# Kernel optimization log

Measured on AMD Instinct MI355X. Metric: run time of the kernel, lower is better.

## Reference

```python
import jax, jax.numpy as jnp
import numpy as np
import math

C_IN, C_OUT = 256, 256
KH, KW = 3, 3
STRIDE, PAD = 1, 1
CURV = 1.0
SQRT_C = math.sqrt(CURV)
EPS = 1e-15

def _beta(a, b):
    return math.exp(math.lgamma(a) + math.lgamma(b) - math.lgamma(a + b))

BETA_NI = _beta(C_IN / 2.0, 0.5)                 # beta(n_i/2, 1/2)
BETA_N = _beta(C_IN * KH * KW / 2.0, 0.5)        # beta(n/2, 1/2)


def logmap0(y, axis):
    n = jnp.maximum(jnp.linalg.norm(y, axis=axis, keepdims=True), EPS)
    return jnp.arctanh(jnp.minimum(SQRT_C * n, 1.0 - 1e-7)) * y / (SQRT_C * n)


def expmap0(v, axis):
    n = jnp.maximum(jnp.linalg.norm(v, axis=axis, keepdims=True), EPS)
    return jnp.tanh(SQRT_C * n) * v / (SQRT_C * n)


def unfold(x):
    # torch.nn.Unfold: x [B,C,H,W] -> [B, C*KH*KW, L], channel-major patch order
    B, C, H, W = x.shape
    Ho = (H + 2 * PAD - KH) // STRIDE + 1
    Wo = (W + 2 * PAD - KW) // STRIDE + 1
    xp = jnp.pad(x, ((0, 0), (0, 0), (PAD, PAD), (PAD, PAD)))
    cols = [xp[:, :, i:i + STRIDE * Ho:STRIDE, j:j + STRIDE * Wo:STRIDE]
            for i in range(KH) for j in range(KW)]
    patches = jnp.stack(cols, axis=2)            # [B, C, KH*KW, Ho, Wo]
    return patches.reshape(B, C * KH * KW, Ho * Wo), Ho, Wo


def poincare_fc(x, z, r):
    # x: [..., D_in] on ball, z: [D_in, D_out], r: [D_out]
    x2 = jnp.sum(x * x, axis=-1, keepdims=True)
    lam = 2.0 / (1.0 - CURV * x2)                # conformal factor lambda_x
    z_norm = jnp.maximum(jnp.linalg.norm(z, axis=0), EPS)  # [D_out]
    xz = x @ z                                   # [..., D_out]
    two_csr = 2.0 * SQRT_C * r
    inner = (SQRT_C * lam * xz / z_norm * jnp.cosh(two_csr)
             - (lam - 1.0) * jnp.sinh(two_csr))
    v = 2.0 * z_norm / SQRT_C * jnp.arcsinh(inner)   # hyperplane distances
    w = jnp.sinh(SQRT_C * v) / SQRT_C
    return w / (1.0 + jnp.sqrt(1.0 + CURV * jnp.sum(w * w, axis=-1, keepdims=True)))


def setup_inputs() -> dict:
    key = jax.random.key(0)
    k1, k2, k3 = jax.random.split(key, 3)
    # tangent vectors -> points on the Poincare ball (man_dim=1)
    v = 0.05 * jax.random.normal(k1, (16, C_IN, 64, 64), dtype=jnp.float32)
    x = expmap0(v, axis=1)
    std = (2.0 * C_IN * KH * KW * C_OUT) ** (-0.5)
    weights = std * jax.random.normal(k2, (KH * KW * C_IN, C_OUT), dtype=jnp.float32)
    bias = 0.01 * jax.random.normal(k3, (C_OUT,), dtype=jnp.float32)
    return {"x": x, "weights": weights, "bias": bias}


def reference(x, weights, bias):
    B = x.shape[0]
    v = logmap0(x, axis=1) * (BETA_N / BETA_NI)      # log map + beta scaling
    u, Ho, Wo = unfold(v)                            # [B, CK, L]
    u = jnp.swapaxes(u, 1, 2)                        # [B, L, CK]
    p = expmap0(u, axis=-1)                          # back onto the ball
    y = poincare_fc(p, weights, bias)                # [B, L, C_OUT]
    return jnp.swapaxes(y, 1, 2).reshape(B, C_OUT, Ho, Wo)
```

## Files before the change

### kernel.cpp

```cpp
#include <hip/hip_runtime.h>
#include <cmath>

typedef __bf16 bf16;
typedef __bf16 bf16x8 __attribute__((ext_vector_type(8)));
typedef float f32x4 __attribute__((ext_vector_type(4)));

#define SBAR() __builtin_amdgcn_sched_barrier(0)


__device__ inline void gload16(const void* g, void* l) {
    __builtin_amdgcn_global_load_lds(
        (const __attribute__((address_space(1))) unsigned int*)g,
        (__attribute__((address_space(3))) unsigned int*)l, 16, 0, 0);
}

__global__ void k_prep_zt(const float* __restrict__ z, bf16* __restrict__ zt5) {
    int s = blockIdx.x;
    int cc = s / 9, tap = s % 9;
    int co = threadIdx.x;
#pragma unroll
    for (int g = 0; g < 4; ++g) {
        bf16x8 pk;
#pragma unroll
        for (int e = 0; e < 8; ++e) {
            int c = cc * 32 + g * 8 + e;
            pk[e] = (bf16)z[(size_t)(c * 9 + tap) * 256 + co];
        }
        *(bf16x8*)(zt5 + ((size_t)(s * 4 + g) * 256 + co) * 8) = pk;
    }
}

__global__ void k_prep_cols(const float* __restrict__ z, const float* __restrict__ r,
                            float* __restrict__ zn, float* __restrict__ ch,
                            float* __restrict__ sh) {
    __shared__ float red[256];
    int co = blockIdx.x, t = threadIdx.x;
    float s = 0.f;
    for (int i = 0; i < 9; ++i) {
        float v = z[(size_t)(i * 256 + t) * 256 + co];
        s += v * v;
    }
    red[t] = s;
    __syncthreads();
    for (int off = 128; off >= 1; off >>= 1) {
        if (t < off) red[t] += red[t + off];
        __syncthreads();
    }
    if (t == 0) {
        zn[co] = fmaxf(sqrtf(red[0]), 1e-15f);
        float tc = 2.f * r[co];
        ch[co] = coshf(tc);
        sh[co] = sinhf(tc);
    }
}

__global__ void k_logmap(const float* __restrict__ x, unsigned int* __restrict__ vt_u,
                         float* __restrict__ sq, float Rbeta) {
    __shared__ float tile[256][33];
    __shared__ float red[8][32];
    __shared__ float afac[32];
    int tid = threadIdx.x;
    int blk = blockIdx.x;
    int b = blk >> 7;
    int pix0 = (blk & 127) << 5;

    for (int it = 0; it < 32; ++it) {
        int c = it * 8 + (tid >> 5);
        int p = tid & 31;
        tile[c][p] = x[((size_t)b * 256 + c) * 4096 + pix0 + p];
    }
    __syncthreads();

    {
        int part = tid >> 5, p = tid & 31;
        float s = 0.f;
        for (int i = 0; i < 32; ++i) {
            float v = tile[part * 32 + i][p];
            s += v * v;
        }
        red[part][p] = s;
    }
    __syncthreads();
    if (tid < 32) {
        float n2 = 0.f;
        for (int i = 0; i < 8; ++i) n2 += red[i][tid];
        float n = sqrtf(n2);
        float nc = fmaxf(n, 1e-15f);
        float a = atanhf(fminf(nc, 0.9999999f)) / nc * Rbeta;
        afac[tid] = a;
        sq[(size_t)b * 4096 + pix0 + tid] = a * a * n2;
    }
    __syncthreads();

    for (int it = 0; it < 16; ++it) {
        int idx = it * 256 + tid;
        int p = idx >> 7;
        int cp = idx & 127;
        float a = afac[p];
        float v0 = a * tile[2 * cp][p];
        float v1 = a * tile[2 * cp + 1][p];
        union { bf16 h[2]; unsigned int u; } pk;
        pk.h[0] = (bf16)v0;
        pk.h[1] = (bf16)v1;
        vt_u[((size_t)b * 4096 + pix0 + p) * 128 + cp] = pk.u;
    }
}

__global__ void k_boxsum(const float* __restrict__ sq, float* __restrict__ nusq) {
    int idx = blockIdx.x * 256 + threadIdx.x;
    int b = idx >> 12, hw = idx & 4095, h = hw >> 6, w = hw & 63;
    const float* s = sq + ((size_t)b << 12);
    float acc = 0.f;
    for (int dh = -1; dh <= 1; ++dh) {
        int hh = h + dh;
        if ((unsigned)hh >= 64u) continue;
        for (int dw = -1; dw <= 1; ++dw) {
            int ww = w + dw;
            if ((unsigned)ww >= 64u) continue;
            acc += s[hh * 64 + ww];
        }
    }
    nusq[idx] = acc;
}

__global__ void
__attribute__((amdgpu_flat_work_group_size(512, 512)))
__attribute__((amdgpu_waves_per_eu(4, 4)))
k_hconv(const bf16* __restrict__ vt, const bf16* __restrict__ zt5,
        const float* __restrict__ nusq,
        const float* __restrict__ znp, const float* __restrict__ chp,
        const float* __restrict__ shp, float* __restrict__ out) {
    __shared__ __align__(1024) char Asb[16896];
    __shared__ __align__(1024) char Bsb[3][16448];
    __shared__ float s_lds[128], lam_lds[128];
    __shared__ float red[128][4];

    int tid = threadIdx.x;
    int bid = blockIdx.x;
    int bh = ((bid & 7) << 6) | (bid >> 3);
    int b = bh >> 5, h0 = (bh & 31) << 1;

    if (tid < 32) {
        int u = tid >> 1, side = tid & 1;
        *(f32x4*)(Asb + u * 1056 + side * 1040) = (f32x4){0.f, 0.f, 0.f, 0.f};
    }

    if (tid >= 128 && tid < 256) {
        int t = tid - 128;
        int h = h0 + (t >> 6), w = t & 63;
        float q = nusq[((size_t)b << 12) + h * 64 + w];
        float ncl = fmaxf(sqrtf(q), 1e-15f);
        float p = __expf(2.f * ncl);
        float tt = (p - 1.f) / (p + 1.f);
        s_lds[t] = tt / ncl;
        lam_lds[t] = 2.f / (1.f - tt * tt);
    }

    int wave = tid >> 6, lane = tid & 63;
    int wn = wave & 3, wm = wave >> 2;
    int lrow = lane & 15, lk = lane >> 4;

    f32x4 acc[4][4];
#pragma unroll
    for (int m = 0; m < 4; ++m)
#pragma unroll
        for (int n = 0; n < 4; ++n) acc[m][n] = (f32x4){0.f, 0.f, 0.f, 0.f};

    const bf16* vb = vt + (((size_t)b) << 12) * 256;

    auto stageA = [&](int ccn) {
#pragma unroll
        for (int it = 0; it < 2; ++it) {
            int u = wave * 2 + it;
            int r = u >> 2, g = u & 3;
            int hr = h0 - 1 + r;
            hr = hr < 0 ? 0 : (hr > 63 ? 63 : hr);
            const bf16* gp = vb + ((size_t)(hr * 64 + lane)) * 256 + ccn * 32 + g * 8;
            gload16(gp, Asb + u * 1056 + 16);
        }
    };
    auto stageB = [&](char* dst, int snext) {
        const char* src = (const char*)zt5 + (size_t)snext * 16384;
#pragma unroll
        for (int it = 0; it < 2; ++it) {
            int u = wave * 2 + it;
            gload16(src + u * 1024 + lane * 16,
                    dst + (u >> 2) * 4112 + (u & 3) * 1024);
        }
    };

    stageB((char*)Bsb[0], 0);
    stageA(0);
    __syncthreads();
    SBAR();

    const char* ApB = Asb + lk * 1056 + lrow * 16;
    const int bOff = lk * 4112 + wn * 1024 + lrow * 16;

#pragma unroll 1
    for (int cc = 0; cc < 8; ++cc) {
        const int sbase = cc * 9;
        const bool notlast = (cc < 7);

#pragma unroll
        for (int tap = 0; tap < 9; ++tap) {
            const int s = sbase + tap;
            if (s < 71) stageB((char*)Bsb[(tap + 1) % 3], s + 1);
            SBAR();
            if (s < 71) { asm volatile("s_waitcnt vmcnt(2)" ::: "memory"); }
            else        { asm volatile("s_waitcnt vmcnt(0)" ::: "memory"); }
            SBAR();
            asm volatile("s_barrier" ::: "memory");
            SBAR();

            const int dh = tap / 3 - 1, dw = tap % 3 - 1;
            int hh = h0 + wm + dh;
            if ((unsigned)hh < 64u) {
                const char* Ap = ApB + (wm + dh + 1) * 4224 + (dw + 1) * 16;
                const char* Bp = (const char*)Bsb[tap % 3] + bOff;
                bf16x8 a0 = *(const bf16x8*)(Ap);
                bf16x8 a1 = *(const bf16x8*)(Ap + 256);
                bf16x8 a2 = *(const bf16x8*)(Ap + 512);
                bf16x8 a3 = *(const bf16x8*)(Ap + 768);
                bf16x8 b0 = *(const bf16x8*)(Bp);
                bf16x8 b1 = *(const bf16x8*)(Bp + 256);
                bf16x8 b2 = *(const bf16x8*)(Bp + 512);
                bf16x8 b3 = *(const bf16x8*)(Bp + 768);
                __builtin_amdgcn_s_setprio(1);
                acc[0][0] = __builtin_amdgcn_mfma_f32_16x16x32_bf16(a0, b0, acc[0][0], 0, 0, 0);
                acc[1][0] = __builtin_amdgcn_mfma_f32_16x16x32_bf16(a1, b0, acc[1][0], 0, 0, 0);
                acc[2][0] = __builtin_amdgcn_mfma_f32_16x16x32_bf16(a2, b0, acc[2][0], 0, 0, 0);
                acc[3][0] = __builtin_amdgcn_mfma_f32_16x16x32_bf16(a3, b0, acc[3][0], 0, 0, 0);
                acc[0][1] = __builtin_amdgcn_mfma_f32_16x16x32_bf16(a0, b1, acc[0][1], 0, 0, 0);
                acc[1][1] = __builtin_amdgcn_mfma_f32_16x16x32_bf16(a1, b1, acc[1][1], 0, 0, 0);
                acc[2][1] = __builtin_amdgcn_mfma_f32_16x16x32_bf16(a2, b1, acc[2][1], 0, 0, 0);
                acc[3][1] = __builtin_amdgcn_mfma_f32_16x16x32_bf16(a3, b1, acc[3][1], 0, 0, 0);
                acc[0][2] = __builtin_amdgcn_mfma_f32_16x16x32_bf16(a0, b2, acc[0][2], 0, 0, 0);
                acc[1][2] = __builtin_amdgcn_mfma_f32_16x16x32_bf16(a1, b2, acc[1][2], 0, 0, 0);
                acc[2][2] = __builtin_amdgcn_mfma_f32_16x16x32_bf16(a2, b2, acc[2][2], 0, 0, 0);
                acc[3][2] = __builtin_amdgcn_mfma_f32_16x16x32_bf16(a3, b2, acc[3][2], 0, 0, 0);
                acc[0][3] = __builtin_amdgcn_mfma_f32_16x16x32_bf16(a0, b3, acc[0][3], 0, 0, 0);
                acc[1][3] = __builtin_amdgcn_mfma_f32_16x16x32_bf16(a1, b3, acc[1][3], 0, 0, 0);
                acc[2][3] = __builtin_amdgcn_mfma_f32_16x16x32_bf16(a2, b3, acc[2][3], 0, 0, 0);
                acc[3][3] = __builtin_amdgcn_mfma_f32_16x16x32_bf16(a3, b3, acc[3][3], 0, 0, 0);
                __builtin_amdgcn_s_setprio(0);
            }
            SBAR();
            if (tap == 8) {
                asm volatile("s_barrier" ::: "memory");
                SBAR();
                if (notlast) stageA(cc + 1);
                SBAR();
            }
        }
    }

    float cz[4], sh4[4], tz[4];
#pragma unroll
    for (int n = 0; n < 4; ++n) {
        int co = wn * 64 + n * 16 + lrow;
        float zn = znp[co];
        cz[n] = chp[co] / zn;
        sh4[n] = shp[co];
        tz[n] = 2.f * zn;
    }

#pragma unroll
    for (int m = 0; m < 4; ++m) {
#pragma unroll
        for (int r = 0; r < 4; ++r) {
            int wp = wm * 64 + m * 16 + 4 * lk + r;
            float s = s_lds[wp], lam = lam_lds[wp];
            float lm1 = lam - 1.f;
            float psum = 0.f;
#pragma unroll
            for (int n = 0; n < 4; ++n) {
                float xz = s * acc[m][n][r];
                float inner = lam * xz * cz[n] - lm1 * sh4[n];
                float as = __logf(inner + sqrtf(inner * inner + 1.f));
                float p = __expf(tz[n] * as);
                float w = 0.5f * (p - __builtin_amdgcn_rcpf(p));
                acc[m][n][r] = w;
                psum += w * w;
            }
            psum += __shfl_xor(psum, 1);
            psum += __shfl_xor(psum, 2);
            psum += __shfl_xor(psum, 4);
            psum += __shfl_xor(psum, 8);
            if (lrow == 0) red[wp][wn] = psum;
        }
    }
    __syncthreads();

    float dinv[4][4];
#pragma unroll
    for (int m = 0; m < 4; ++m)
#pragma unroll
        for (int r = 0; r < 4; ++r) {
            int wp = wm * 64 + m * 16 + 4 * lk + r;
            float tot = (red[wp][0] + red[wp][1]) + (red[wp][2] + red[wp][3]);
            dinv[m][r] = __builtin_amdgcn_rcpf(1.f + sqrtf(1.f + tot));
        }

    float* ob = out + (size_t)b * 256 * 4096 + (h0 + wm) * 64;
#pragma unroll
    for (int m = 0; m < 4; ++m) {
#pragma unroll
        for (int n = 0; n < 4; ++n) {
            int co = wn * 64 + n * 16 + lrow;
            f32x4 o;
#pragma unroll
            for (int r = 0; r < 4; ++r) o[r] = acc[m][n][r] * dinv[m][r];
            *(f32x4*)(ob + (size_t)co * 4096 + m * 16 + 4 * lk) = o;
        }
    }
}

extern "C" void kernel_launch(void* const* d_in, const int* in_sizes, int n_in,
                              void* d_out, int out_size, void* d_ws, size_t ws_size,
                              hipStream_t stream) {
    const float* x = (const float*)d_in[0];
    const float* z = (const float*)d_in[1];
    const float* r = (const float*)d_in[2];
    float* out = (float*)d_out;

    char* ws = (char*)d_ws;
    bf16* vt = (bf16*)ws;
    float* sq = (float*)(ws + 33554432);
    float* nusq = (float*)(ws + 33816576);
    bf16* zt5 = (bf16*)(ws + 34078720);
    float* zn = (float*)(ws + 35258368);
    float* ch = (float*)(ws + 35259392);
    float* sh = (float*)(ws + 35260416);
    if (ws_size < 35261440) return;

    double bni = lgamma(128.0) + lgamma(0.5) - lgamma(128.5);
    double bn = lgamma(1152.0) + lgamma(0.5) - lgamma(1152.5);
    float Rbeta = (float)exp(bn - bni);

    k_prep_zt<<<72, 256, 0, stream>>>(z, zt5);
    k_prep_cols<<<256, 256, 0, stream>>>(z, r, zn, ch, sh);
    k_logmap<<<2048, 256, 0, stream>>>(x, (unsigned int*)vt, sq, Rbeta);
    k_boxsum<<<256, 256, 0, stream>>>(sq, nusq);
    k_hconv<<<512, 512, 0, stream>>>(vt, zt5, nusq, zn, ch, sh, out);
}
```

Before: 127.3 us.

## Load conv A operands directly from global in channel-group-blocked layout, dropping LDS staging

The logmap kernel now writes activations in a channel-group-blocked layout ([B][32 groups][pixel][8 channels]), so each MFMA lane can fetch its 16-byte A fragment straight from global memory. The conv kernel removes the A shared-memory tile and its extra barrier per channel chunk. It prefetches the next tap's A fragments into registers, with border pixels handled by masking lanes to zero. This trades LDS traffic and a sync for more global/L2 loads (each element is re-read across taps) and more vmcnt bookkeeping, and it also pads the B LDS stride differently.

```diff
diff --git a/kernel.cpp b/kernel.cpp
--- a/kernel.cpp
+++ b/kernel.cpp
@@ -94,15 +94,17 @@
 
     for (int it = 0; it < 16; ++it) {
         int idx = it * 256 + tid;
-        int p = idx >> 7;
-        int cp = idx & 127;
+        int q = idx & 3;
+        int p = (idx >> 2) & 31;
+        int g = idx >> 7;
+        int cp = g * 4 + q;
         float a = afac[p];
         float v0 = a * tile[2 * cp][p];
         float v1 = a * tile[2 * cp + 1][p];
         union { bf16 h[2]; unsigned int u; } pk;
         pk.h[0] = (bf16)v0;
         pk.h[1] = (bf16)v1;
-        vt_u[((size_t)b * 4096 + pix0 + p) * 128 + cp] = pk.u;
+        vt_u[((size_t)(b * 32 + g) * 4096 + pix0 + p) * 4 + q] = pk.u;
     }
 }
 
@@ -126,12 +128,11 @@
 __global__ void
 __attribute__((amdgpu_flat_work_group_size(512, 512)))
 __attribute__((amdgpu_waves_per_eu(4, 4)))
-k_hconv(const bf16* __restrict__ vt, const bf16* __restrict__ zt5,
+k_hconv(const bf16* __restrict__ vt2, const bf16* __restrict__ zt5,
         const float* __restrict__ nusq,
         const float* __restrict__ znp, const float* __restrict__ chp,
         const float* __restrict__ shp, float* __restrict__ out) {
-    __shared__ __align__(1024) char Asb[16896];
-    __shared__ __align__(1024) char Bsb[3][16448];
+    __shared__ __align__(1024) char Bsb[3][16512];
     __shared__ float s_lds[128], lam_lds[128];
     __shared__ float red[128][4];
 
@@ -140,20 +141,14 @@
     int bh = ((bid & 7) << 6) | (bid >> 3);
     int b = bh >> 5, h0 = (bh & 31) << 1;
 
-    if (tid < 32) {
-        int u = tid >> 1, side = tid & 1;
-        *(f32x4*)(Asb + u * 1056 + side * 1040) = (f32x4){0.f, 0.f, 0.f, 0.f};
-    }
-
-    if (tid >= 128 && tid < 256) {
-        int t = tid - 128;
-        int h = h0 + (t >> 6), w = t & 63;
+    if (tid < 128) {
+        int h = h0 + (tid >> 6), w = tid & 63;
         float q = nusq[((size_t)b << 12) + h * 64 + w];
         float ncl = fmaxf(sqrtf(q), 1e-15f);
         float p = __expf(2.f * ncl);
         float tt = (p - 1.f) / (p + 1.f);
-        s_lds[t] = tt / ncl;
-        lam_lds[t] = 2.f / (1.f - tt * tt);
+        s_lds[tid] = tt / ncl;
+        lam_lds[tid] = 2.f / (1.f - tt * tt);
     }
 
     int wave = tid >> 6, lane = tid & 63;
@@ -166,49 +161,66 @@
 #pragma unroll
         for (int n = 0; n < 4; ++n) acc[m][n] = (f32x4){0.f, 0.f, 0.f, 0.f};
 
-    const bf16* vb = vt + (((size_t)b) << 12) * 256;
-
-    auto stageA = [&](int ccn) {
+    bf16x8 zf;
+#pragma unroll
+    for (int e = 0; e < 8; ++e) zf[e] = (bf16)0.0f;
+
+    const bf16* Aptr[3];
+#pragma unroll
+    for (int j = 0; j < 3; ++j) {
+        int hj = h0 + wm - 1 + j;
+        hj = hj < 0 ? 0 : (hj > 63 ? 63 : hj);
+        Aptr[j] = vt2 + (size_t)(b * 32 + lk) * 32768 + hj * 512 + lrow * 8;
+    }
+    const int dL = (lrow == 0) ? 0 : -16;
+    const bool okL = (lrow != 0);
+    const bool okR = (lrow != 15);
+
+    auto stageB = [&](char* dst, int snext) {
 #pragma unroll
         for (int it = 0; it < 2; ++it) {
             int u = wave * 2 + it;
-            int r = u >> 2, g = u & 3;
-            int hr = h0 - 1 + r;
-            hr = hr < 0 ? 0 : (hr > 63 ? 63 : hr);
-            const bf16* gp = vb + ((size_t)(hr * 64 + lane)) * 256 + ccn * 32 + g * 8;
-            gload16(gp, Asb + u * 1056 + 16);
+            gload16((const char*)zt5 + (size_t)snext * 16384 + u * 1024 + lane * 16,
+                    dst + (u >> 2) * 4128 + (u & 3) * 1024);
         }
     };
-    auto stageB = [&](char* dst, int snext) {
-        const char* src = (const char*)zt5 + (size_t)snext * 16384;
-#pragma unroll
-        for (int it = 0; it < 2; ++it) {
-            int u = wave * 2 + it;
-            gload16(src + u * 1024 + lane * 16,
-                    dst + (u >> 2) * 4112 + (u & 3) * 1024);
-        }
-    };
 
     stageB((char*)Bsb[0], 0);
-    stageA(0);
+    bf16x8 ap[4];
+#pragma unroll
+    for (int m = 0; m < 4; ++m)
+        ap[m] = (m == 0) ? *(const bf16x8*)((const char*)Aptr[0] + dL)
+                         : *(const bf16x8*)(Aptr[0] + (m * 16 - 1) * 8);
     __syncthreads();
     SBAR();
 
-    const char* ApB = Asb + lk * 1056 + lrow * 16;
-    const int bOff = lk * 4112 + wn * 1024 + lrow * 16;
+    const int bOff = lk * 4128 + wn * 1024 + lrow * 16;
 
 #pragma unroll 1
     for (int cc = 0; cc < 8; ++cc) {
-        const int sbase = cc * 9;
-        const bool notlast = (cc < 7);
-
 #pragma unroll
         for (int tap = 0; tap < 9; ++tap) {
-            const int s = sbase + tap;
-            if (s < 71) stageB((char*)Bsb[(tap + 1) % 3], s + 1);
+            const int s = cc * 9 + tap;
+            const bool lastS = (s == 71);
+
+            if (tap == 8) {
+#pragma unroll
+                for (int j = 0; j < 3; ++j) Aptr[j] += 4 * 32768;
+            }
+            if (!lastS) stageB((char*)Bsb[(tap + 1) % 3], s + 1);
+            bf16x8 an[4];
+            {
+                const int nt = (tap == 8) ? 0 : tap + 1;
+                const int ndh = nt / 3 - 1, ndw = nt % 3 - 1, nj = ndh + 1;
+#pragma unroll
+                for (int m = 0; m < 4; ++m)
+                    an[m] = (ndw == -1 && m == 0)
+                        ? *(const bf16x8*)((const char*)Aptr[nj] + dL)
+                        : *(const bf16x8*)(Aptr[nj] + (m * 16 + ndw) * 8);
+            }
             SBAR();
-            if (s < 71) { asm volatile("s_waitcnt vmcnt(2)" ::: "memory"); }
-            else        { asm volatile("s_waitcnt vmcnt(0)" ::: "memory"); }
+            if (!lastS) { asm volatile("s_waitcnt vmcnt(6)" ::: "memory"); }
+            else        { asm volatile("s_waitcnt vmcnt(4)" ::: "memory"); }
             SBAR();
             asm volatile("s_barrier" ::: "memory");
             SBAR();
@@ -216,12 +228,10 @@
             const int dh = tap / 3 - 1, dw = tap % 3 - 1;
             int hh = h0 + wm + dh;
             if ((unsigned)hh < 64u) {
-                const char* Ap = ApB + (wm + dh + 1) * 4224 + (dw + 1) * 16;
+                bf16x8 a0 = ap[0], a1 = ap[1], a2 = ap[2], a3 = ap[3];
+                if (dw == -1) a0 = okL ? a0 : zf;
+                if (dw == 1)  a3 = okR ? a3 : zf;
                 const char* Bp = (const char*)Bsb[tap % 3] + bOff;
-                bf16x8 a0 = *(const bf16x8*)(Ap);
-                bf16x8 a1 = *(const bf16x8*)(Ap + 256);
-                bf16x8 a2 = *(const bf16x8*)(Ap + 512);
-                bf16x8 a3 = *(const bf16x8*)(Ap + 768);
                 bf16x8 b0 = *(const bf16x8*)(Bp);
                 bf16x8 b1 = *(const bf16x8*)(Bp + 256);
                 bf16x8 b2 = *(const bf16x8*)(Bp + 512);
@@ -246,12 +256,8 @@
                 __builtin_amdgcn_s_setprio(0);
             }
             SBAR();
-            if (tap == 8) {
-                asm volatile("s_barrier" ::: "memory");
-                SBAR();
-                if (notlast) stageA(cc + 1);
-                SBAR();
-            }
+#pragma unroll
+            for (int m = 0; m < 4; ++m) ap[m] = an[m];
         }
     }
 
@@ -325,7 +331,7 @@
     float* out = (float*)d_out;
 
     char* ws = (char*)d_ws;
-    bf16* vt = (bf16*)ws;
+    bf16* vt2 = (bf16*)ws;
     float* sq = (float*)(ws + 33554432);
     float* nusq = (float*)(ws + 33816576);
     bf16* zt5 = (bf16*)(ws + 34078720);
@@ -340,7 +346,7 @@
 
     k_prep_zt<<<72, 256, 0, stream>>>(z, zt5);
     k_prep_cols<<<256, 256, 0, stream>>>(z, r, zn, ch, sh);
-    k_logmap<<<2048, 256, 0, stream>>>(x, (unsigned int*)vt, sq, Rbeta);
+    k_logmap<<<2048, 256, 0, stream>>>(x, (unsigned int*)vt2, sq, Rbeta);
     k_boxsum<<<256, 256, 0, stream>>>(sq, nusq);
-    k_hconv<<<512, 512, 0, stream>>>(vt, zt5, nusq, zn, ch, sh, out);
-}
+    k_hconv<<<512, 512, 0, stream>>>(vt2, zt5, nusq, zn, ch, sh, out);
+}
```

Result: slower. 141.0 us (+10.8%).

## Load weight fragments directly into registers, dropping LDS B staging and per-tap barriers

Applied to the files above, without the earlier changes.

The weight matrix is re-laid out so each lane's four k-groups are contiguous, and the conv kernel now loads its B fragments straight from global memory into double-buffered registers instead of staging them through a triple-buffered LDS ring. This removes the per-tap workgroup barrier and the B LDS traffic. Barriers remain only at channel-chunk boundaries for the A tile. In exchange, every wave issues its own global/L2 reads of the weights, and register pressure rises under the fixed 4-waves-per-EU budget.

```diff
diff --git a/kernel.cpp b/kernel.cpp
--- a/kernel.cpp
+++ b/kernel.cpp
@@ -14,7 +14,7 @@
         (__attribute__((address_space(3))) unsigned int*)l, 16, 0, 0);
 }
 
-__global__ void k_prep_zt(const float* __restrict__ z, bf16* __restrict__ zt5) {
+__global__ void k_prep_zt(const float* __restrict__ z, bf16* __restrict__ zt6) {
     int s = blockIdx.x;
     int cc = s / 9, tap = s % 9;
     int co = threadIdx.x;
@@ -26,7 +26,7 @@
             int c = cc * 32 + g * 8 + e;
             pk[e] = (bf16)z[(size_t)(c * 9 + tap) * 256 + co];
         }
-        *(bf16x8*)(zt5 + ((size_t)(s * 4 + g) * 256 + co) * 8) = pk;
+        *(bf16x8*)(zt6 + ((size_t)(s * 256 + co) * 4 + g) * 8) = pk;
     }
 }
 
@@ -126,12 +126,11 @@
 __global__ void
 __attribute__((amdgpu_flat_work_group_size(512, 512)))
 __attribute__((amdgpu_waves_per_eu(4, 4)))
-k_hconv(const bf16* __restrict__ vt, const bf16* __restrict__ zt5,
+k_hconv(const bf16* __restrict__ vt, const bf16* __restrict__ zt6,
         const float* __restrict__ nusq,
         const float* __restrict__ znp, const float* __restrict__ chp,
         const float* __restrict__ shp, float* __restrict__ out) {
     __shared__ __align__(1024) char Asb[16896];
-    __shared__ __align__(1024) char Bsb[3][16448];
     __shared__ float s_lds[128], lam_lds[128];
     __shared__ float red[128][4];
 
@@ -179,81 +178,85 @@
             gload16(gp, Asb + u * 1056 + 16);
         }
     };
-    auto stageB = [&](char* dst, int snext) {
-        const char* src = (const char*)zt5 + (size_t)snext * 16384;
-#pragma unroll
-        for (int it = 0; it < 2; ++it) {
-            int u = wave * 2 + it;
-            gload16(src + u * 1024 + lane * 16,
-                    dst + (u >> 2) * 4112 + (u & 3) * 1024);
-        }
-    };
-
-    stageB((char*)Bsb[0], 0);
+
+    const bf16* bp = zt6 + ((size_t)(wn * 64 + lrow) * 4 + lk) * 8;
+    bf16x8 bA[4], bB[4];
+#pragma unroll
+    for (int n = 0; n < 4; ++n) bA[n] = *(const bf16x8*)(bp + n * 512);
+    const bf16* bnp = bp + 8192;
+
     stageA(0);
     __syncthreads();
     SBAR();
 
     const char* ApB = Asb + lk * 1056 + lrow * 16;
-    const int bOff = lk * 4112 + wn * 1024 + lrow * 16;
+
+#define STAGE(CCV, TAP, CUR, NXT)                                            \
+    {                                                                        \
+        const int s_ = (CCV) * 9 + (TAP);                                    \
+        if (s_ < 71) {                                                       \
+            NXT[0] = *(const bf16x8*)(bnp);                                  \
+            NXT[1] = *(const bf16x8*)(bnp + 512);                            \
+            NXT[2] = *(const bf16x8*)(bnp + 1024);                           \
+            NXT[3] = *(const bf16x8*)(bnp + 1536);                           \
+            bnp += 8192;                                                     \
+        }                                                                    \
+        SBAR();                                                              \
+        if ((TAP) == 0) {                                                    \
+            asm volatile("s_waitcnt vmcnt(4)" ::: "memory");                 \
+            SBAR();                                                          \
+            asm volatile("s_barrier" ::: "memory");         \
+            SBAR();                                                          \
+        }                                                                    \
+        {                                                                    \
+            const int dh_ = (TAP) / 3 - 1, dw_ = (TAP) % 3 - 1;              \
+            int hh_ = h0 + wm + dh_;                                         \
+            if ((unsigned)hh_ < 64u) {                                       \
+                const char* Ap_ = ApB + (wm + dh_ + 1) * 4224 + (dw_ + 1) * 16; \
+                bf16x8 a0 = *(const bf16x8*)(Ap_);                           \
+                bf16x8 a1 = *(const bf16x8*)(Ap_ + 256);                     \
+                bf16x8 a2 = *(const bf16x8*)(Ap_ + 512);                     \
+                bf16x8 a3 = *(const bf16x8*)(Ap_ + 768);                     \
+                __builtin_amdgcn_s_setprio(1);                               \
+                acc[0][0] = __builtin_amdgcn_mfma_f32_16x16x32_bf16(a0, CUR[0], acc[0][0], 0, 0, 0); \
+                acc[1][0] = __builtin_amdgcn_mfma_f32_16x16x32_bf16(a1, CUR[0], acc[1][0], 0, 0, 0); \
+                acc[2][0] = __builtin_amdgcn_mfma_f32_16x16x32_bf16(a2, CUR[0], acc[2][0], 0, 0, 0); \
+                acc[3][0] = __builtin_amdgcn_mfma_f32_16x16x32_bf16(a3, CUR[0], acc[3][0], 0, 0, 0); \
+                acc[0][1] = __builtin_amdgcn_mfma_f32_16x16x32_bf16(a0, CUR[1], acc[0][1], 0, 0, 0); \
+                acc[1][1] = __builtin_amdgcn_mfma_f32_16x16x32_bf16(a1, CUR[1], acc[1][1], 0, 0, 0); \
+                acc[2][1] = __builtin_amdgcn_mfma_f32_16x16x32_bf16(a2, CUR[1], acc[2][1], 0, 0, 0); \
+                acc[3][1] = __builtin_amdgcn_mfma_f32_16x16x32_bf16(a3, CUR[1], acc[3][1], 0, 0, 0); \
+                acc[0][2] = __builtin_amdgcn_mfma_f32_16x16x32_bf16(a0, CUR[2], acc[0][2], 0, 0, 0); \
+                acc[1][2] = __builtin_amdgcn_mfma_f32_16x16x32_bf16(a1, CUR[2], acc[1][2], 0, 0, 0); \
+                acc[2][2] = __builtin_amdgcn_mfma_f32_16x16x32_bf16(a2, CUR[2], acc[2][2], 0, 0, 0); \
+                acc[3][2] = __builtin_amdgcn_mfma_f32_16x16x32_bf16(a3, CUR[2], acc[3][2], 0, 0, 0); \
+                acc[0][3] = __builtin_amdgcn_mfma_f32_16x16x32_bf16(a0, CUR[3], acc[0][3], 0, 0, 0); \
+                acc[1][3] = __builtin_amdgcn_mfma_f32_16x16x32_bf16(a1, CUR[3], acc[1][3], 0, 0, 0); \
+                acc[2][3] = __builtin_amdgcn_mfma_f32_16x16x32_bf16(a2, CUR[3], acc[2][3], 0, 0, 0); \
+                acc[3][3] = __builtin_amdgcn_mfma_f32_16x16x32_bf16(a3, CUR[3], acc[3][3], 0, 0, 0); \
+                __builtin_amdgcn_s_setprio(0);                               \
+            }                                                                \
+        }                                                                    \
+        SBAR();                                                              \
+        if ((TAP) == 8 && (CCV) < 7) {                                       \
+            asm volatile("s_barrier" ::: "memory");    \
+            SBAR();                                                          \
+            stageA((CCV) + 1);                                               \
+            SBAR();                                                          \
+        }                                                                    \
+    }
 
 #pragma unroll 1
-    for (int cc = 0; cc < 8; ++cc) {
-        const int sbase = cc * 9;
-        const bool notlast = (cc < 7);
-
-#pragma unroll
-        for (int tap = 0; tap < 9; ++tap) {
-            const int s = sbase + tap;
-            if (s < 71) stageB((char*)Bsb[(tap + 1) % 3], s + 1);
-            SBAR();
-            if (s < 71) { asm volatile("s_waitcnt vmcnt(2)" ::: "memory"); }
-            else        { asm volatile("s_waitcnt vmcnt(0)" ::: "memory"); }
-            SBAR();
-            asm volatile("s_barrier" ::: "memory");
-            SBAR();
-
-            const int dh = tap / 3 - 1, dw = tap % 3 - 1;
-            int hh = h0 + wm + dh;
-            if ((unsigned)hh < 64u) {
-                const char* Ap = ApB + (wm + dh + 1) * 4224 + (dw + 1) * 16;
-                const char* Bp = (const char*)Bsb[tap % 3] + bOff;
-                bf16x8 a0 = *(const bf16x8*)(Ap);
-                bf16x8 a1 = *(const bf16x8*)(Ap + 256);
-                bf16x8 a2 = *(const bf16x8*)(Ap + 512);
-                bf16x8 a3 = *(const bf16x8*)(Ap + 768);
-                bf16x8 b0 = *(const bf16x8*)(Bp);
-                bf16x8 b1 = *(const bf16x8*)(Bp + 256);
-                bf16x8 b2 = *(const bf16x8*)(Bp + 512);
-                bf16x8 b3 = *(const bf16x8*)(Bp + 768);
-                __builtin_amdgcn_s_setprio(1);
-                acc[0][0] = __builtin_amdgcn_mfma_f32_16x16x32_bf16(a0, b0, acc[0][0], 0, 0, 0);
-                acc[1][0] = __builtin_amdgcn_mfma_f32_16x16x32_bf16(a1, b0, acc[1][0], 0, 0, 0);
-                acc[2][0] = __builtin_amdgcn_mfma_f32_16x16x32_bf16(a2, b0, acc[2][0], 0, 0, 0);
-                acc[3][0] = __builtin_amdgcn_mfma_f32_16x16x32_bf16(a3, b0, acc[3][0], 0, 0, 0);
-                acc[0][1] = __builtin_amdgcn_mfma_f32_16x16x32_bf16(a0, b1, acc[0][1], 0, 0, 0);
-                acc[1][1] = __builtin_amdgcn_mfma_f32_16x16x32_bf16(a1, b1, acc[1][1], 0, 0, 0);
-                acc[2][1] = __builtin_amdgcn_mfma_f32_16x16x32_bf16(a2, b1, acc[2][1], 0, 0, 0);
-                acc[3][1] = __builtin_amdgcn_mfma_f32_16x16x32_bf16(a3, b1, acc[3][1], 0, 0, 0);
-                acc[0][2] = __builtin_amdgcn_mfma_f32_16x16x32_bf16(a0, b2, acc[0][2], 0, 0, 0);
-                acc[1][2] = __builtin_amdgcn_mfma_f32_16x16x32_bf16(a1, b2, acc[1][2], 0, 0, 0);
-                acc[2][2] = __builtin_amdgcn_mfma_f32_16x16x32_bf16(a2, b2, acc[2][2], 0, 0, 0);
-                acc[3][2] = __builtin_amdgcn_mfma_f32_16x16x32_bf16(a3, b2, acc[3][2], 0, 0, 0);
-                acc[0][3] = __builtin_amdgcn_mfma_f32_16x16x32_bf16(a0, b3, acc[0][3], 0, 0, 0);
-                acc[1][3] = __builtin_amdgcn_mfma_f32_16x16x32_bf16(a1, b3, acc[1][3], 0, 0, 0);
-                acc[2][3] = __builtin_amdgcn_mfma_f32_16x16x32_bf16(a2, b3, acc[2][3], 0, 0, 0);
-                acc[3][3] = __builtin_amdgcn_mfma_f32_16x16x32_bf16(a3, b3, acc[3][3], 0, 0, 0);
-                __builtin_amdgcn_s_setprio(0);
-            }
-            SBAR();
-            if (tap == 8) {
-                asm volatile("s_barrier" ::: "memory");
-                SBAR();
-                if (notlast) stageA(cc + 1);
-                SBAR();
-            }
-        }
-    }
+    for (int cc2 = 0; cc2 < 4; ++cc2) {
+        const int c0 = cc2 * 2, c1 = c0 + 1;
+        STAGE(c0, 0, bA, bB) STAGE(c0, 1, bB, bA) STAGE(c0, 2, bA, bB)
+        STAGE(c0, 3, bB, bA) STAGE(c0, 4, bA, bB) STAGE(c0, 5, bB, bA)
+        STAGE(c0, 6, bA, bB) STAGE(c0, 7, bB, bA) STAGE(c0, 8, bA, bB)
+        STAGE(c1, 0, bB, bA) STAGE(c1, 1, bA, bB) STAGE(c1, 2, bB, bA)
+        STAGE(c1, 3, bA, bB) STAGE(c1, 4, bB, bA) STAGE(c1, 5, bA, bB)
+        STAGE(c1, 6, bB, bA) STAGE(c1, 7, bA, bB) STAGE(c1, 8, bB, bA)
+    }
+#undef STAGE
 
     float cz[4], sh4[4], tz[4];
 #pragma unroll
@@ -328,7 +331,7 @@
     bf16* vt = (bf16*)ws;
     float* sq = (float*)(ws + 33554432);
     float* nusq = (float*)(ws + 33816576);
-    bf16* zt5 = (bf16*)(ws + 34078720);
+    bf16* zt6 = (bf16*)(ws + 34078720);
     float* zn = (float*)(ws + 35258368);
     float* ch = (float*)(ws + 35259392);
     float* sh = (float*)(ws + 35260416);
@@ -338,9 +341,9 @@
     double bn = lgamma(1152.0) + lgamma(0.5) - lgamma(1152.5);
     float Rbeta = (float)exp(bn - bni);
 
-    k_prep_zt<<<72, 256, 0, stream>>>(z, zt5);
+    k_prep_zt<<<72, 256, 0, stream>>>(z, zt6);
     k_prep_cols<<<256, 256, 0, stream>>>(z, r, zn, ch, sh);
     k_logmap<<<2048, 256, 0, stream>>>(x, (unsigned int*)vt, sq, Rbeta);
     k_boxsum<<<256, 256, 0, stream>>>(sq, nusq);
-    k_hconv<<<512, 512, 0, stream>>>(vt, zt5, nusq, zn, ch, sh, out);
-}
+    k_hconv<<<512, 512, 0, stream>>>(vt, zt6, nusq, zn, ch, sh, out);
+}
```

After: 131.3 us. 3.2% more time.
